# Kernel optimization log

Measured on AMD Instinct MI355X. Metric: run time of the kernel, lower is better.

## Reference

```python
import jax, jax.numpy as jnp
import numpy as np

N_NODES = 100000
N_EDGES = 600000
D = 128
N_TYPES = 3


def setup_inputs() -> dict:
    key = jax.random.key(0)
    ks = jax.random.split(key, 10)
    x = jax.random.normal(ks[0], (N_NODES, D), dtype=jnp.float32)
    edge_index = jax.random.randint(ks[1], (2, N_EDGES), 0, N_NODES, dtype=jnp.int64)
    edge_type_ids = jax.random.randint(ks[2], (N_EDGES,), 0, N_TYPES, dtype=jnp.int32)
    edge_weights = jax.random.uniform(ks[3], (N_EDGES,), dtype=jnp.float32)
    # Xavier-uniform linear weights (in==out==D), zero biases, uniform attention
    limit = float(np.sqrt(6.0 / (D + D)))
    W_edge = jax.random.uniform(ks[4], (N_TYPES, D, D), minval=-limit, maxval=limit, dtype=jnp.float32)
    b_edge = jnp.zeros((N_TYPES, D), dtype=jnp.float32)
    W_self = jax.random.uniform(ks[5], (D, D), minval=-limit, maxval=limit, dtype=jnp.float32)
    b_self = jnp.zeros((D,), dtype=jnp.float32)
    attention = jnp.ones((N_TYPES + 1,), dtype=jnp.float32) / (N_TYPES + 1)
    return {"x": x, "edge_index": edge_index, "edge_type_ids": edge_type_ids,
            "edge_weights": edge_weights, "W_edge": W_edge, "b_edge": b_edge,
            "W_self": W_self, "b_self": b_self, "attention": attention}


def reference(x, edge_index, edge_type_ids, edge_weights, W_edge, b_edge, W_self, b_self, attention):
    n_nodes = x.shape[0]
    n_types = W_edge.shape[0]
    src, dst = edge_index[0], edge_index[1]
    xs = x[src]  # (E, D) gather once, shared by all edge types
    outs = []
    for t in range(n_types):  # small fixed set of structurally distinct linears
        # mask zeros out edges of other types; equivalent to torch's boolean slicing
        m = jnp.where(edge_type_ids == t, edge_weights, jnp.zeros((), x.dtype))
        y = (xs @ W_edge[t] + b_edge[t]) * m[:, None]  # (E, D)
        outs.append(jax.ops.segment_sum(y, dst, num_segments=n_nodes))  # scatter-add
    outs.append(x @ W_self + b_self)
    stacked = jnp.stack(outs, axis=-1)  # (N, D, n_types+1)
    attn = jax.nn.softmax(attention)
    out = jnp.sum(stacked * attn, axis=-1)
    return jax.nn.gelu(out, approximate=False)  # torch F.gelu default is erf-based
```

## Files before the change

kernel.cpp:

```cpp
#include <hip/hip_runtime.h>
#include <hip/hip_bf16.h>
#include <math.h>

#define D 128
#define NT 3
#define KTOT (D * (NT + 1))
#define TM 32
#define NCAP 32

typedef __attribute__((ext_vector_type(8))) __bf16 bf16x8;
typedef __attribute__((ext_vector_type(4))) float f32x4;

__device__ inline unsigned short f2bf(float f) {
    unsigned int u = __float_as_uint(f);
    unsigned int r = (u + 0x7FFFu + ((u >> 16) & 1u)) >> 16;
    return (unsigned short)r;
}
__device__ inline float bf2f(unsigned int low16) {
    return __uint_as_float(low16 << 16);
}

__global__ void zero_kernel(float* __restrict__ p, long long n4) {
    long long i = (long long)blockIdx.x * blockDim.x + threadIdx.x;
    long long stride = (long long)gridDim.x * blockDim.x;
    float4 z = make_float4(0.f, 0.f, 0.f, 0.f);
    for (; i < n4; i += stride) ((float4*)p)[i] = z;
}

__global__ void prep_kernel(const float* __restrict__ W_edge, const float* __restrict__ b_edge,
                            const float* __restrict__ W_self, const float* __restrict__ b_self,
                            const float* __restrict__ attention,
                            float* __restrict__ wcat, float* __restrict__ biasb,
                            unsigned short* __restrict__ bfrag,
                            int* __restrict__ zeroMe, int zeroN) {
    float a0 = attention[0], a1 = attention[1], a2 = attention[2], a3 = attention[3];
    float m = fmaxf(fmaxf(a0, a1), fmaxf(a2, a3));
    float e0 = expf(a0 - m), e1 = expf(a1 - m), e2 = expf(a2 - m), e3 = expf(a3 - m);
    float inv = 1.f / (e0 + e1 + e2 + e3);
    float at[4] = {e0 * inv, e1 * inv, e2 * inv, e3 * inv};

    int idx0 = blockIdx.x * blockDim.x + threadIdx.x;
    int stride = gridDim.x * blockDim.x;
    if (zeroMe) {
        for (int i = idx0; i < zeroN; i += stride) zeroMe[i] = 0;
    }
    for (int i = idx0; i < KTOT * D; i += stride) {
        int k = i >> 7, j = i & (D - 1);
        float v;
        if (k < D) {
            v = at[NT] * W_self[k * D + j];
        } else {
            int t = (k - D) >> 7;
            int kk = (k - D) & (D - 1);
            v = at[t] * W_edge[(t * D + kk) * D + j];
        }
        wcat[i] = v;
    }
    for (int i = idx0; i < KTOT; i += stride) {
        if (i < NT * D) {
            int t = i >> 7, j = i & (D - 1);
            biasb[i] = at[t] * b_edge[t * D + j];
        } else {
            biasb[i] = at[NT] * b_self[i - NT * D];
        }
    }
    if (bfrag) {
        for (int i = idx0; i < 16 * 8 * 64; i += stride) {
            int l = i & 63;
            int cf = (i >> 6) & 7;
            int step = i >> 9;
            int col = cf * 16 + (l & 15);
            int kb = step * 32 + ((l >> 4) * 8);
#pragma unroll
            for (int j = 0; j < 8; ++j) {
                int k = kb + j;
                float v;
                if (k < D) {
                    v = at[NT] * W_self[k * D + col];
                } else {
                    int t = (k - D) >> 7;
                    int kk = (k - D) & (D - 1);
                    v = at[t] * W_edge[(t * D + kk) * D + col];
                }
                bfrag[(size_t)i * 8 + j] = f2bf(v);
            }
        }
    }
}

__global__ __launch_bounds__(256) void xcvt_fill_kernel(
    const float* __restrict__ x, unsigned short* __restrict__ xb, int nN,
    const int* __restrict__ ei, const int* __restrict__ et, const float* __restrict__ ew,
    int* __restrict__ deg, int2* __restrict__ csr, int* __restrict__ ovfcnt,
    int* __restrict__ ovflist, int nE) {
    int e = blockIdx.x * blockDim.x + threadIdx.x;

    int dst = 0, src = 0, t = 0;
    float w = 0.f;
    bool act = (e < nE);
    if (act) {
        dst = ei[nE + e];
        src = ei[e];
        t = et[e];
        w = ew[e];
    }

    int total = nN * (D / 4);
    int stride = gridDim.x * blockDim.x;
    for (int i = e; i < total; i += stride) {
        int n = i >> 5;
        int c4 = (i & 31) * 4;
        float4 v = *(const float4*)(x + (size_t)n * D + c4);
        ushort4 o;
        o.x = f2bf(v.x); o.y = f2bf(v.y); o.z = f2bf(v.z); o.w = f2bf(v.w);
        *(ushort4*)(xb + (size_t)n * D + c4) = o;
    }

    if (act) {
        int pos = atomicAdd(deg + dst, 1);
        if (pos < NCAP) {
            csr[(size_t)dst * NCAP + pos] = make_int2(src | (t << 20), __float_as_int(w));
        } else {
            int o = atomicAdd(ovfcnt, 1);
            ovflist[o] = e;
        }
    }
}

__global__ __launch_bounds__(512, 8) void fused_gemm_kernel(
    const unsigned short* __restrict__ xb, const int2* __restrict__ csr,
    const int* __restrict__ deg, const unsigned short* __restrict__ bfrag,
    const float* __restrict__ biasb,
    const int* __restrict__ ei, const int* __restrict__ et, const float* __restrict__ ew,
    const int* __restrict__ ovfc, const int* __restrict__ ovfl,
    float* __restrict__ out, int nN, int nE) {
    __shared__ unsigned char lds[33152];
    float* sL = (float*)(lds + 32768);
    int t = threadIdx.x;
    int w = t >> 6;
    int lane = t & 63;
    int gl = lane & 15;
    int gbase = lane & 48;
    int row0 = blockIdx.x * TM;

    int lrow = w * 4 + (lane >> 4);
    int node = row0 + lrow;
    int nclamp = (node < nN) ? node : (nN - 1);
    int dg = (node < nN) ? deg[nclamp] : 0;
    if (dg > NCAP) dg = NCAP;
    const int2* c = csr + (size_t)nclamp * NCAP;
    int2 mA = (gl < dg) ? c[gl] : make_int2(0, 0);
    int2 mB = (gl + 16 < dg) ? c[gl + 16] : make_int2(0, 0);

    float ac0[8], ac1[8], ac2[8];
#pragma unroll
    for (int j = 0; j < 8; ++j) { ac0[j] = 0.f; ac1[j] = 0.f; ac2[j] = 0.f; }
    float sw0 = 0.f, sw1 = 0.f, sw2 = 0.f;

    for (int i = 0; i < dg; i += 2) {
        int slA = gbase + (i & 15);
        int exA = __shfl((i < 16) ? mA.x : mB.x, slA);
        int ewA = __shfl((i < 16) ? mA.y : mB.y, slA);
        int srcA = exA & 0xFFFFF;
        if (srcA >= nN) srcA = 0;
        float wA = __int_as_float(ewA);
        int tA = (exA >> 20) & 3;
        bool actB = (i + 1 < dg);
        int slB = gbase + ((i + 1) & 15);
        int exB = __shfl((i + 1 < 16) ? mA.x : mB.x, slB);
        int ewB = __shfl((i + 1 < 16) ? mA.y : mB.y, slB);
        int srcB = exB & 0xFFFFF;
        if (!actB || srcB >= nN) srcB = 0;
        float wB = actB ? __int_as_float(ewB) : 0.f;
        int tB = (exB >> 20) & 3;

        uint4 xa = *(const uint4*)(xb + (size_t)srcA * D + gl * 8);
        uint4 xv = *(const uint4*)(xb + (size_t)srcB * D + gl * 8);

        float wA0 = (tA == 0) ? wA : 0.f;
        float wA1 = (tA == 1) ? wA : 0.f;
        float wA2 = (tA == 2) ? wA : 0.f;
        float wB0 = (tB == 0) ? wB : 0.f;
        float wB1 = (tB == 1) ? wB : 0.f;
        float wB2 = (tB == 2) ? wB : 0.f;
        sw0 += wA0 + wB0; sw1 += wA1 + wB1; sw2 += wA2 + wB2;

        float f0, f1;
#define ACCUM(u, j0, j1, w0_, w1_, w2_)                                   \
        f0 = __uint_as_float((u) << 16);                                  \
        f1 = __uint_as_float((u) & 0xFFFF0000u);                          \
        ac0[j0] = fmaf(w0_, f0, ac0[j0]); ac0[j1] = fmaf(w0_, f1, ac0[j1]); \
        ac1[j0] = fmaf(w1_, f0, ac1[j0]); ac1[j1] = fmaf(w1_, f1, ac1[j1]); \
        ac2[j0] = fmaf(w2_, f0, ac2[j0]); ac2[j1] = fmaf(w2_, f1, ac2[j1]);
        ACCUM(xa.x, 0, 1, wA0, wA1, wA2)
        ACCUM(xa.y, 2, 3, wA0, wA1, wA2)
        ACCUM(xa.z, 4, 5, wA0, wA1, wA2)
        ACCUM(xa.w, 6, 7, wA0, wA1, wA2)
        ACCUM(xv.x, 0, 1, wB0, wB1, wB2)
        ACCUM(xv.y, 2, 3, wB0, wB1, wB2)
        ACCUM(xv.z, 4, 5, wB0, wB1, wB2)
        ACCUM(xv.w, 6, 7, wB0, wB1, wB2)
#undef ACCUM
    }

    {
        int swz = lrow & 15;
        uint4 xo = *(const uint4*)(xb + (size_t)nclamp * D + gl * 8);
        *(uint4*)(lds + lrow * 1024 + ((gl ^ swz) << 4)) = xo;
        uint4 o;
#define PACKST(arr, tt)                                                                \
        o.x = (unsigned int)f2bf(arr[0]) | ((unsigned int)f2bf(arr[1]) << 16);         \
        o.y = (unsigned int)f2bf(arr[2]) | ((unsigned int)f2bf(arr[3]) << 16);         \
        o.z = (unsigned int)f2bf(arr[4]) | ((unsigned int)f2bf(arr[5]) << 16);         \
        o.w = (unsigned int)f2bf(arr[6]) | ((unsigned int)f2bf(arr[7]) << 16);         \
        *(uint4*)(lds + lrow * 1024 + 256 + (tt) * 256 + ((gl ^ swz) << 4)) = o;
        PACKST(ac0, 0)
        PACKST(ac1, 1)
        PACKST(ac2, 2)
#undef PACKST
        if (gl < 3) {
            float sv = (gl == 0) ? sw0 : ((gl == 1) ? sw1 : sw2);
            sL[lrow * NT + gl] = sv;
        }
    }
    __syncthreads();

    int cnt = *ovfc;
    if (cnt > 0) {
        if (w == 0 && lane < 16) {
            for (int i = 0; i < cnt; ++i) {
                int e = ovfl[i];
                int dst = ei[nE + e];
                if (dst >= row0 && dst < row0 + TM && dst < nN) {
                    int tt = et[e];
                    float wt = ew[e];
                    int src = ei[e];
                    int lr = dst - row0;
                    uint4* p = (uint4*)(lds + lr * 1024 + 256 + tt * 256 + ((lane ^ (lr & 15)) << 4));
                    uint4 cu = *p;
                    uint4 xr = *(const uint4*)(xb + (size_t)src * D + lane * 8);
                    float f0 = bf2f(cu.x & 0xFFFF) + wt * bf2f(xr.x & 0xFFFF);
                    float f1 = bf2f(cu.x >> 16)    + wt * bf2f(xr.x >> 16);
                    float f2 = bf2f(cu.y & 0xFFFF) + wt * bf2f(xr.y & 0xFFFF);
                    float f3 = bf2f(cu.y >> 16)    + wt * bf2f(xr.y >> 16);
                    float f4 = bf2f(cu.z & 0xFFFF) + wt * bf2f(xr.z & 0xFFFF);
                    float f5 = bf2f(cu.z >> 16)    + wt * bf2f(xr.z >> 16);
                    float f6 = bf2f(cu.w & 0xFFFF) + wt * bf2f(xr.w & 0xFFFF);
                    float f7 = bf2f(cu.w >> 16)    + wt * bf2f(xr.w >> 16);
                    cu.x = (unsigned int)f2bf(f0) | ((unsigned int)f2bf(f1) << 16);
                    cu.y = (unsigned int)f2bf(f2) | ((unsigned int)f2bf(f3) << 16);
                    cu.z = (unsigned int)f2bf(f4) | ((unsigned int)f2bf(f5) << 16);
                    cu.w = (unsigned int)f2bf(f6) | ((unsigned int)f2bf(f7) << 16);
                    *p = cu;
                    if (lane == 0) sL[lr * NT + tt] += wt;
                }
            }
        }
        __syncthreads();
    }

    int ll = lane & 15;
    int ck = lane >> 4;
    f32x4 acc0 = (f32x4){0.f, 0.f, 0.f, 0.f};
    f32x4 acc1 = (f32x4){0.f, 0.f, 0.f, 0.f};
#pragma unroll 4
    for (int st = 0; st < 16; ++st) {
        bf16x8 b = *(const bf16x8*)(bfrag + (size_t)st * 4096 + w * 512 + lane * 8);
        int cc = st * 4 + ck;
        int phys = (cc & 48) | ((cc & 15) ^ ll);
        bf16x8 a0 = *(const bf16x8*)(lds + ll * 1024 + (phys << 4));
        bf16x8 a1 = *(const bf16x8*)(lds + (16 + ll) * 1024 + (phys << 4));
        acc0 = __builtin_amdgcn_mfma_f32_16x16x32_bf16(a0, b, acc0, 0, 0, 0);
        acc1 = __builtin_amdgcn_mfma_f32_16x16x32_bf16(a1, b, acc1, 0, 0, 0);
    }

    int colb = w * 16 + ll;
    float bb0 = biasb[colb], bb1 = biasb[D + colb], bb2 = biasb[2 * D + colb], bs4 = biasb[3 * D + colb];
    const float kInvSqrt2 = 0.70710678118654752440f;
#pragma unroll
    for (int fr = 0; fr < 2; ++fr) {
        f32x4 A = fr ? acc1 : acc0;
#pragma unroll
        for (int reg = 0; reg < 4; ++reg) {
            int lr = fr * 16 + ck * 4 + reg;
            long row = (long)row0 + lr;
            if (row >= nN) continue;
            float s0 = sL[lr * NT + 0];
            float s1 = sL[lr * NT + 1];
            float s2 = sL[lr * NT + 2];
            float v = A[reg] + bs4 + s0 * bb0 + s1 * bb1 + s2 * bb2;
            v = 0.5f * v * (1.f + erff(v * kInvSqrt2));
            out[row * D + colb] = v;
        }
    }
}

__global__ __launch_bounds__(256) void scatterA_kernel(
    const float* __restrict__ x, const int* __restrict__ ei,
    const int* __restrict__ et, const float* __restrict__ ew,
    float* __restrict__ agg, float* __restrict__ s, int nE) {
    int gtid = blockIdx.x * blockDim.x + threadIdx.x;
    int wave = gtid >> 6;
    int lane = threadIdx.x & 63;
    int nw = (gridDim.x * blockDim.x) >> 6;
    for (int e = wave; e < nE; e += nw) {
        int src = ei[e];
        int dst = ei[nE + e];
        int t = et[e];
        float w = ew[e];
        float2 xv = *(const float2*)(x + (size_t)src * D + lane * 2);
        float* p = agg + (size_t)dst * (NT * D) + t * D + lane * 2;
        unsafeAtomicAdd(p, w * xv.x);
        unsafeAtomicAdd(p + 1, w * xv.y);
        if (lane == 0) unsafeAtomicAdd(s + (size_t)dst * NT + t, w);
    }
}

#define BM 64
#define BK 32
__global__ __launch_bounds__(256) void gemm_gelu_kernel(
    const float* __restrict__ x, const float* __restrict__ agg,
    const float* __restrict__ s, const float* __restrict__ wcat,
    const float* __restrict__ biasb, float* __restrict__ out, int nNodes) {
    __shared__ float As[BK][BM + 1];
    __shared__ float Bs[BK][D];

    int tx = threadIdx.x;
    int row0 = blockIdx.x * BM;
    int cg = tx & 31;
    int rg = tx >> 5;
    int lr = tx >> 3;
    int lc = (tx & 7) * 4;

    float acc[8][4];
#pragma unroll
    for (int i = 0; i < 8; ++i)
#pragma unroll
        for (int j = 0; j < 4; ++j) acc[i][j] = 0.f;

    for (int k0 = 0; k0 < KTOT; k0 += BK) {
        const float* srcBase;
        int strideA, koff;
        if (k0 < D) { srcBase = x; strideA = D; koff = k0; }
        else        { srcBase = agg; strideA = NT * D; koff = k0 - D; }
#pragma unroll
        for (int h = 0; h < 2; ++h) {
            int r = lr + h * 32;
            int node = row0 + r;
            if (node >= nNodes) node = nNodes - 1;
            float4 v = *(const float4*)(srcBase + (size_t)node * strideA + koff + lc);
            As[lc + 0][r] = v.x; As[lc + 1][r] = v.y;
            As[lc + 2][r] = v.z; As[lc + 3][r] = v.w;
        }
        {
            int br = tx >> 5;
            int bc = (tx & 31) * 4;
#pragma unroll
            for (int h = 0; h < 4; ++h) {
                int r = br + h * 8;
                *(float4*)(&Bs[r][bc]) = *(const float4*)(wcat + (size_t)(k0 + r) * D + bc);
            }
        }
        __syncthreads();
#pragma unroll
        for (int kk = 0; kk < BK; ++kk) {
            float4 b = *(const float4*)(&Bs[kk][cg * 4]);
            float a[8];
            *(float4*)(a)     = *(const float4*)(&As[kk][rg * 8]);
            *(float4*)(a + 4) = *(const float4*)(&As[kk][rg * 8 + 4]);
#pragma unroll
            for (int i = 0; i < 8; ++i) {
                acc[i][0] = fmaf(a[i], b.x, acc[i][0]);
                acc[i][1] = fmaf(a[i], b.y, acc[i][1]);
                acc[i][2] = fmaf(a[i], b.z, acc[i][2]);
                acc[i][3] = fmaf(a[i], b.w, acc[i][3]);
            }
        }
        __syncthreads();
    }

    int jc = cg * 4;
    float4 bb0 = *(const float4*)(biasb + 0 * D + jc);
    float4 bb1 = *(const float4*)(biasb + 1 * D + jc);
    float4 bb2 = *(const float4*)(biasb + 2 * D + jc);
    float4 bsv = *(const float4*)(biasb + NT * D + jc);
#pragma unroll
    for (int i = 0; i < 8; ++i) {
        int node = row0 + rg * 8 + i;
        if (node >= nNodes) break;
        float s0 = s[(size_t)node * NT + 0];
        float s1 = s[(size_t)node * NT + 1];
        float s2 = s[(size_t)node * NT + 2];
        float4 r;
        r.x = acc[i][0] + bsv.x + s0 * bb0.x + s1 * bb1.x + s2 * bb2.x;
        r.y = acc[i][1] + bsv.y + s0 * bb0.y + s1 * bb1.y + s2 * bb2.y;
        r.z = acc[i][2] + bsv.z + s0 * bb0.z + s1 * bb1.z + s2 * bb2.z;
        r.w = acc[i][3] + bsv.w + s0 * bb0.w + s1 * bb1.w + s2 * bb2.w;
        const float kInvSqrt2 = 0.70710678118654752440f;
        r.x = 0.5f * r.x * (1.f + erff(r.x * kInvSqrt2));
        r.y = 0.5f * r.y * (1.f + erff(r.y * kInvSqrt2));
        r.z = 0.5f * r.z * (1.f + erff(r.z * kInvSqrt2));
        r.w = 0.5f * r.w * (1.f + erff(r.w * kInvSqrt2));
        *(float4*)(out + (size_t)node * D + jc) = r;
    }
}

__global__ __launch_bounds__(256) void selfmv_kernel(
    const float* __restrict__ x, const float* __restrict__ Ws,
    const float* __restrict__ bs, const float* __restrict__ attn,
    float* __restrict__ out, int nN) {
    float a0 = attn[0], a1 = attn[1], a2 = attn[2], a3 = attn[3];
    float m = fmaxf(fmaxf(a0, a1), fmaxf(a2, a3));
    float e3 = expf(a3 - m);
    float inv = 1.f / (expf(a0 - m) + expf(a1 - m) + expf(a2 - m) + e3);
    float at3 = e3 * inv;
    int wave = (blockIdx.x * blockDim.x + threadIdx.x) >> 6;
    int lane = threadIdx.x & 63;
    int nw = (gridDim.x * blockDim.x) >> 6;
    for (int n = wave; n < nN; n += nw) {
        float2 xr = *(const float2*)(x + (size_t)n * D + lane * 2);
        float acc0 = 0.f, acc1 = 0.f;
#pragma unroll
        for (int k = 0; k < D; ++k) {
            float xv = __shfl((k & 1) ? xr.y : xr.x, k >> 1);
            float2 wv = *(const float2*)(Ws + (size_t)k * D + lane * 2);
            acc0 = fmaf(xv, wv.x, acc0);
            acc1 = fmaf(xv, wv.y, acc1);
        }
        float2 r;
        r.x = at3 * (acc0 + bs[lane * 2]);
        r.y = at3 * (acc1 + bs[lane * 2 + 1]);
        *(float2*)(out + (size_t)n * D + lane * 2) = r;
    }
}

__global__ __launch_bounds__(256) void edgemv_kernel(
    const float* __restrict__ x, const int* __restrict__ ei,
    const int* __restrict__ et, const float* __restrict__ ew,
    const float* __restrict__ We, const float* __restrict__ be,
    const float* __restrict__ attn, float* __restrict__ out, int nE) {
    float a0 = attn[0], a1 = attn[1], a2 = attn[2], a3 = attn[3];
    float m = fmaxf(fmaxf(a0, a1), fmaxf(a2, a3));
    float e0 = expf(a0 - m), e1 = expf(a1 - m), e2 = expf(a2 - m), e3 = expf(a3 - m);
    float inv = 1.f / (e0 + e1 + e2 + e3);
    float at[NT] = {e0 * inv, e1 * inv, e2 * inv};
    int wave = (blockIdx.x * blockDim.x + threadIdx.x) >> 6;
    int lane = threadIdx.x & 63;
    int nw = (gridDim.x * blockDim.x) >> 6;
    for (int e = wave; e < nE; e += nw) {
        int src = ei[e];
        int dst = ei[nE + e];
        int t = et[e];
        float sc = ew[e] * at[t];
        const float* W = We + (size_t)t * D * D;
        float2 xr = *(const float2*)(x + (size_t)src * D + lane * 2);
        float acc0 = 0.f, acc1 = 0.f;
#pragma unroll
        for (int k = 0; k < D; ++k) {
            float xv = __shfl((k & 1) ? xr.y : xr.x, k >> 1);
            float2 wv = *(const float2*)(W + (size_t)k * D + lane * 2);
            acc0 = fmaf(xv, wv.x, acc0);
            acc1 = fmaf(xv, wv.y, acc1);
        }
        float* p = out + (size_t)dst * D + lane * 2;
        unsafeAtomicAdd(p,     sc * (acc0 + be[(size_t)t * D + lane * 2]));
        unsafeAtomicAdd(p + 1, sc * (acc1 + be[(size_t)t * D + lane * 2 + 1]));
    }
}

__global__ void gelu_kernel(float* __restrict__ p, long long n4) {
    long long i = (long long)blockIdx.x * blockDim.x + threadIdx.x;
    long long stride = (long long)gridDim.x * blockDim.x;
    const float kInvSqrt2 = 0.70710678118654752440f;
    for (; i < n4; i += stride) {
        float4 r = ((float4*)p)[i];
        r.x = 0.5f * r.x * (1.f + erff(r.x * kInvSqrt2));
        r.y = 0.5f * r.y * (1.f + erff(r.y * kInvSqrt2));
        r.z = 0.5f * r.z * (1.f + erff(r.z * kInvSqrt2));
        r.w = 0.5f * r.w * (1.f + erff(r.w * kInvSqrt2));
        ((float4*)p)[i] = r;
    }
}

extern "C" void kernel_launch(void* const* d_in, const int* in_sizes, int n_in,
                              void* d_out, int out_size, void* d_ws, size_t ws_size,
                              hipStream_t stream) {
    const float* x = (const float*)d_in[0];
    const int* ei = (const int*)d_in[1];
    const int* et = (const int*)d_in[2];
    const float* ew = (const float*)d_in[3];
    const float* W_edge = (const float*)d_in[4];
    const float* b_edge = (const float*)d_in[5];
    const float* W_self = (const float*)d_in[6];
    const float* b_self = (const float*)d_in[7];
    const float* attention = (const float*)d_in[8];
    float* out = (float*)d_out;

    const int nN = in_sizes[0] / D;
    const int nE = in_sizes[2];

    size_t off = 0;
    auto take = [&](size_t bytes) { size_t o = (off + 15) & ~(size_t)15; off = o + bytes; return o; };
    size_t o_wcat  = take((size_t)KTOT * D * 4);
    size_t o_biasb = take((size_t)KTOT * 4);
    size_t o_bfrag = take(131072);
    size_t o_deg   = take((size_t)(nN + 2) * 4);
    size_t o_ovfl  = take((size_t)nE * 4);
    size_t o_csr   = take((size_t)nN * NCAP * 8);
    size_t o_xb    = take((size_t)nN * D * 2);
    size_t needFused = off;

    if (ws_size >= needFused && nN < (1 << 20)) {
        char* ws = (char*)d_ws;
        float* wcat = (float*)(ws + o_wcat);
        float* biasb = (float*)(ws + o_biasb);
        unsigned short* bfrag = (unsigned short*)(ws + o_bfrag);
        int* deg = (int*)(ws + o_deg);
        int* ovfc = deg + nN;
        int* ovfl = (int*)(ws + o_ovfl);
        int2* csr = (int2*)(ws + o_csr);
        unsigned short* xb = (unsigned short*)(ws + o_xb);

        hipLaunchKernelGGL(prep_kernel, dim3(64), dim3(256), 0, stream,
                           W_edge, b_edge, W_self, b_self, attention, wcat, biasb, bfrag,
                           deg, nN + 2);
        hipLaunchKernelGGL(xcvt_fill_kernel, dim3((nE + 255) / 256), dim3(256), 0, stream,
                           x, xb, nN, ei, et, ew, deg, csr, ovfc, ovfl, nE);
        hipLaunchKernelGGL(fused_gemm_kernel, dim3((nN + TM - 1) / TM), dim3(512), 0, stream,
                           xb, csr, deg, bfrag, biasb, ei, et, ew, ovfc, ovfl, out, nN, nE);
        return;
    }

    const size_t baseFloats = (size_t)nN * NT * D + (size_t)nN * NT + (size_t)KTOT * D + KTOT;
    if (ws_size >= baseFloats * 4) {
        float* agg = (float*)d_ws;
        float* sW = agg + (size_t)nN * NT * D;
        float* wcat = sW + (size_t)nN * NT;
        float* biasb = wcat + (size_t)KTOT * D;
        long long zeroFloats = (long long)nN * (NT * D + NT);
        hipLaunchKernelGGL(zero_kernel, dim3(2048), dim3(256), 0, stream, agg, (zeroFloats + 3) / 4);
        hipLaunchKernelGGL(prep_kernel, dim3(64), dim3(256), 0, stream,
                           W_edge, b_edge, W_self, b_self, attention, wcat, biasb,
                           (unsigned short*)nullptr, (int*)nullptr, 0);
        hipLaunchKernelGGL(scatterA_kernel, dim3(2048), dim3(256), 0, stream,
                           x, ei, et, ew, agg, sW, nE);
        hipLaunchKernelGGL(gemm_gelu_kernel, dim3((nN + BM - 1) / BM), dim3(256), 0, stream,
                           x, agg, sW, wcat, biasb, out, nN);
    } else {
        hipLaunchKernelGGL(selfmv_kernel, dim3(2048), dim3(256), 0, stream,
                           x, W_self, b_self, attention, out, nN);
        hipLaunchKernelGGL(edgemv_kernel, dim3(2048), dim3(256), 0, stream,
                           x, ei, et, ew, W_edge, b_edge, attention, out, nE);
        hipLaunchKernelGGL(gelu_kernel, dim3(2048), dim3(256), 0, stream,
                           out, (long long)nN * D / 4);
    }
}
```

Baseline: 117.4 us.

## Bucket CSR adjacency by edge type to drop per-edge type masking

```diff
diff --git a/kernel.cpp b/kernel.cpp
--- a/kernel.cpp
+++ b/kernel.cpp
@@ -6,7 +6,8 @@
 #define NT 3
 #define KTOT (D * (NT + 1))
 #define TM 32
-#define NCAP 32
+#define TCAP 12
+#define NCAP (3 * TCAP)
 
 typedef __attribute__((ext_vector_type(8))) __bf16 bf16x8;
 typedef __attribute__((ext_vector_type(4))) float f32x4;
@@ -91,7 +92,7 @@
 __global__ __launch_bounds__(256) void xcvt_fill_kernel(
     const float* __restrict__ x, unsigned short* __restrict__ xb, int nN,
     const int* __restrict__ ei, const int* __restrict__ et, const float* __restrict__ ew,
-    int* __restrict__ deg, int2* __restrict__ csr, int* __restrict__ ovfcnt,
+    int* __restrict__ deg4, int2* __restrict__ csr, int* __restrict__ ovfcnt,
     int* __restrict__ ovflist, int nE) {
     int e = blockIdx.x * blockDim.x + threadIdx.x;
 
@@ -117,9 +118,9 @@
     }
 
     if (act) {
-        int pos = atomicAdd(deg + dst, 1);
-        if (pos < NCAP) {
-            csr[(size_t)dst * NCAP + pos] = make_int2(src | (t << 20), __float_as_int(w));
+        int pos = atomicAdd(deg4 + (size_t)dst * 4 + t, 1);
+        if (pos < TCAP) {
+            csr[(size_t)dst * NCAP + t * TCAP + pos] = make_int2(src, __float_as_int(w));
         } else {
             int o = atomicAdd(ovfcnt, 1);
             ovflist[o] = e;
@@ -129,7 +130,7 @@
 
 __global__ __launch_bounds__(512, 8) void fused_gemm_kernel(
     const unsigned short* __restrict__ xb, const int2* __restrict__ csr,
-    const int* __restrict__ deg, const unsigned short* __restrict__ bfrag,
+    const int* __restrict__ deg4, const unsigned short* __restrict__ bfrag,
     const float* __restrict__ biasb,
     const int* __restrict__ ei, const int* __restrict__ et, const float* __restrict__ ew,
     const int* __restrict__ ovfc, const int* __restrict__ ovfl,
@@ -146,82 +147,68 @@
     int lrow = w * 4 + (lane >> 4);
     int node = row0 + lrow;
     int nclamp = (node < nN) ? node : (nN - 1);
-    int dg = (node < nN) ? deg[nclamp] : 0;
-    if (dg > NCAP) dg = NCAP;
+    int swz = lrow & 15;
+    int4 dgv = make_int4(0, 0, 0, 0);
+    if (node < nN) dgv = *(const int4*)(deg4 + (size_t)nclamp * 4);
+    int cnt0 = dgv.x > TCAP ? TCAP : dgv.x;
+    int cnt1 = dgv.y > TCAP ? TCAP : dgv.y;
+    int cnt2 = dgv.z > TCAP ? TCAP : dgv.z;
+
     const int2* c = csr + (size_t)nclamp * NCAP;
-    int2 mA = (gl < dg) ? c[gl] : make_int2(0, 0);
-    int2 mB = (gl + 16 < dg) ? c[gl + 16] : make_int2(0, 0);
-
-    float ac0[8], ac1[8], ac2[8];
-#pragma unroll
-    for (int j = 0; j < 8; ++j) { ac0[j] = 0.f; ac1[j] = 0.f; ac2[j] = 0.f; }
-    float sw0 = 0.f, sw1 = 0.f, sw2 = 0.f;
-
-    for (int i = 0; i < dg; i += 2) {
-        int slA = gbase + (i & 15);
-        int exA = __shfl((i < 16) ? mA.x : mB.x, slA);
-        int ewA = __shfl((i < 16) ? mA.y : mB.y, slA);
-        int srcA = exA & 0xFFFFF;
-        if (srcA >= nN) srcA = 0;
-        float wA = __int_as_float(ewA);
-        int tA = (exA >> 20) & 3;
-        bool actB = (i + 1 < dg);
-        int slB = gbase + ((i + 1) & 15);
-        int exB = __shfl((i + 1 < 16) ? mA.x : mB.x, slB);
-        int ewB = __shfl((i + 1 < 16) ? mA.y : mB.y, slB);
-        int srcB = exB & 0xFFFFF;
-        if (!actB || srcB >= nN) srcB = 0;
-        float wB = actB ? __int_as_float(ewB) : 0.f;
-        int tB = (exB >> 20) & 3;
-
-        uint4 xa = *(const uint4*)(xb + (size_t)srcA * D + gl * 8);
-        uint4 xv = *(const uint4*)(xb + (size_t)srcB * D + gl * 8);
-
-        float wA0 = (tA == 0) ? wA : 0.f;
-        float wA1 = (tA == 1) ? wA : 0.f;
-        float wA2 = (tA == 2) ? wA : 0.f;
-        float wB0 = (tB == 0) ? wB : 0.f;
-        float wB1 = (tB == 1) ? wB : 0.f;
-        float wB2 = (tB == 2) ? wB : 0.f;
-        sw0 += wA0 + wB0; sw1 += wA1 + wB1; sw2 += wA2 + wB2;
-
-        float f0, f1;
-#define ACCUM(u, j0, j1, w0_, w1_, w2_)                                   \
-        f0 = __uint_as_float((u) << 16);                                  \
-        f1 = __uint_as_float((u) & 0xFFFF0000u);                          \
-        ac0[j0] = fmaf(w0_, f0, ac0[j0]); ac0[j1] = fmaf(w0_, f1, ac0[j1]); \
-        ac1[j0] = fmaf(w1_, f0, ac1[j0]); ac1[j1] = fmaf(w1_, f1, ac1[j1]); \
-        ac2[j0] = fmaf(w2_, f0, ac2[j0]); ac2[j1] = fmaf(w2_, f1, ac2[j1]);
-        ACCUM(xa.x, 0, 1, wA0, wA1, wA2)
-        ACCUM(xa.y, 2, 3, wA0, wA1, wA2)
-        ACCUM(xa.z, 4, 5, wA0, wA1, wA2)
-        ACCUM(xa.w, 6, 7, wA0, wA1, wA2)
-        ACCUM(xv.x, 0, 1, wB0, wB1, wB2)
-        ACCUM(xv.y, 2, 3, wB0, wB1, wB2)
-        ACCUM(xv.z, 4, 5, wB0, wB1, wB2)
-        ACCUM(xv.w, 6, 7, wB0, wB1, wB2)
-#undef ACCUM
-    }
+    int gli = (gl < TCAP) ? gl : (TCAP - 1);
+    int2 m0 = c[gli];
+    int2 m1 = c[TCAP + gli];
+    int2 m2 = c[2 * TCAP + gli];
 
     {
-        int swz = lrow & 15;
         uint4 xo = *(const uint4*)(xb + (size_t)nclamp * D + gl * 8);
         *(uint4*)(lds + lrow * 1024 + ((gl ^ swz) << 4)) = xo;
-        uint4 o;
-#define PACKST(arr, tt)                                                                \
-        o.x = (unsigned int)f2bf(arr[0]) | ((unsigned int)f2bf(arr[1]) << 16);         \
-        o.y = (unsigned int)f2bf(arr[2]) | ((unsigned int)f2bf(arr[3]) << 16);         \
-        o.z = (unsigned int)f2bf(arr[4]) | ((unsigned int)f2bf(arr[5]) << 16);         \
-        o.w = (unsigned int)f2bf(arr[6]) | ((unsigned int)f2bf(arr[7]) << 16);         \
-        *(uint4*)(lds + lrow * 1024 + 256 + (tt) * 256 + ((gl ^ swz) << 4)) = o;
-        PACKST(ac0, 0)
-        PACKST(ac1, 1)
-        PACKST(ac2, 2)
-#undef PACKST
-        if (gl < 3) {
-            float sv = (gl == 0) ? sw0 : ((gl == 1) ? sw1 : sw2);
-            sL[lrow * NT + gl] = sv;
-        }
+    }
+
+    float sw0 = 0.f, sw1 = 0.f, sw2 = 0.f;
+
+#define ACCP(uA, uB, jj0, jj1)                                                      \
+    aacc[jj0] = fmaf(wA, __uint_as_float((uA) << 16), aacc[jj0]);                   \
+    aacc[jj1] = fmaf(wA, __uint_as_float((uA) & 0xFFFF0000u), aacc[jj1]);           \
+    aacc[jj0] = fmaf(wB, __uint_as_float((uB) << 16), aacc[jj0]);                   \
+    aacc[jj1] = fmaf(wB, __uint_as_float((uB) & 0xFFFF0000u), aacc[jj1]);
+
+#define TYPELOOP(mt, cntt, swt, tt) do {                                            \
+    float aacc[8];                                                                  \
+    _Pragma("unroll") for (int j = 0; j < 8; ++j) aacc[j] = 0.f;                    \
+    for (int i = 0; i < cntt; i += 2) {                                             \
+        int exA = __shfl(mt.x, gbase + i);                                          \
+        int ewA = __shfl(mt.y, gbase + i);                                          \
+        int exB = __shfl(mt.x, gbase + i + 1);                                      \
+        int ewB = __shfl(mt.y, gbase + i + 1);                                      \
+        bool actB = (i + 1 < cntt);                                                 \
+        int srcA = exA; if ((unsigned)srcA >= (unsigned)nN) srcA = 0;               \
+        int srcB = actB ? exB : 0; if ((unsigned)srcB >= (unsigned)nN) srcB = 0;    \
+        float wA = __int_as_float(ewA);                                             \
+        float wB = actB ? __int_as_float(ewB) : 0.f;                                \
+        uint4 xa = *(const uint4*)(xb + (size_t)srcA * D + gl * 8);                 \
+        uint4 xv = *(const uint4*)(xb + (size_t)srcB * D + gl * 8);                 \
+        swt += wA + wB;                                                             \
+        ACCP(xa.x, xv.x, 0, 1) ACCP(xa.y, xv.y, 2, 3)                               \
+        ACCP(xa.z, xv.z, 4, 5) ACCP(xa.w, xv.w, 6, 7)                               \
+    }                                                                               \
+    uint4 o;                                                                        \
+    o.x = (unsigned)f2bf(aacc[0]) | ((unsigned)f2bf(aacc[1]) << 16);                \
+    o.y = (unsigned)f2bf(aacc[2]) | ((unsigned)f2bf(aacc[3]) << 16);                \
+    o.z = (unsigned)f2bf(aacc[4]) | ((unsigned)f2bf(aacc[5]) << 16);                \
+    o.w = (unsigned)f2bf(aacc[6]) | ((unsigned)f2bf(aacc[7]) << 16);                \
+    *(uint4*)(lds + lrow * 1024 + 256 + (tt) * 256 + ((gl ^ swz) << 4)) = o;        \
+} while (0)
+
+    TYPELOOP(m0, cnt0, sw0, 0);
+    TYPELOOP(m1, cnt1, sw1, 1);
+    TYPELOOP(m2, cnt2, sw2, 2);
+#undef TYPELOOP
+#undef ACCP
+
+    if (gl < 3) {
+        float sv = (gl == 0) ? sw0 : ((gl == 1) ? sw1 : sw2);
+        sL[lrow * NT + gl] = sv;
     }
     __syncthreads();
 
@@ -504,7 +491,7 @@
     size_t o_wcat  = take((size_t)KTOT * D * 4);
     size_t o_biasb = take((size_t)KTOT * 4);
     size_t o_bfrag = take(131072);
-    size_t o_deg   = take((size_t)(nN + 2) * 4);
+    size_t o_deg   = take(((size_t)nN * 4 + 2) * 4);
     size_t o_ovfl  = take((size_t)nE * 4);
     size_t o_csr   = take((size_t)nN * NCAP * 8);
     size_t o_xb    = take((size_t)nN * D * 2);
@@ -515,19 +502,19 @@
         float* wcat = (float*)(ws + o_wcat);
         float* biasb = (float*)(ws + o_biasb);
         unsigned short* bfrag = (unsigned short*)(ws + o_bfrag);
-        int* deg = (int*)(ws + o_deg);
-        int* ovfc = deg + nN;
+        int* deg4 = (int*)(ws + o_deg);
+        int* ovfc = deg4 + (size_t)nN * 4;
         int* ovfl = (int*)(ws + o_ovfl);
         int2* csr = (int2*)(ws + o_csr);
         unsigned short* xb = (unsigned short*)(ws + o_xb);
 
         hipLaunchKernelGGL(prep_kernel, dim3(64), dim3(256), 0, stream,
                            W_edge, b_edge, W_self, b_self, attention, wcat, biasb, bfrag,
-                           deg, nN + 2);
+                           deg4, nN * 4 + 2);
         hipLaunchKernelGGL(xcvt_fill_kernel, dim3((nE + 255) / 256), dim3(256), 0, stream,
-                           x, xb, nN, ei, et, ew, deg, csr, ovfc, ovfl, nE);
+                           x, xb, nN, ei, et, ew, deg4, csr, ovfc, ovfl, nE);
         hipLaunchKernelGGL(fused_gemm_kernel, dim3((nN + TM - 1) / TM), dim3(512), 0, stream,
-                           xb, csr, deg, bfrag, biasb, ei, et, ew, ovfc, ovfl, out, nN, nE);
+                           xb, csr, deg4, bfrag, biasb, ei, et, ew, ovfc, ovfl, out, nN, nE);
         return;
     }
 
```

After: 123.3 us. +5.1%, slower.
